# Optimization experiments

Measured on AMD Instinct MI355X. Metric: run time of the kernel, lower is better.

Reference implementation:

```python
import jax, jax.numpy as jnp
import numpy as np

B, D, C = 4096, 128, 256


def setup_inputs() -> dict:
    key = jax.random.key(0)
    kx, km, kc = jax.random.split(key, 3)
    X = jax.random.normal(kx, (B, D), dtype=jnp.float32)
    means = jax.random.normal(km, (D, C), dtype=jnp.float32)
    # Build an SPD covariance and invert it (as the torch module does in __init__)
    A = jax.random.normal(kc, (D, D), dtype=jnp.float32)
    covar = A @ A.T / D + jnp.eye(D, dtype=jnp.float32)
    alpha = jnp.linalg.inv(covar)  # [D, D]
    return {"X": X, "means": means, "alpha": alpha}


def reference(X, means, alpha):
    # X: [B, D], means: [D, C], alpha: [D, D]
    d2 = X[:, :, None] - means[None, :, :]          # [B, D, C]
    # Quadratic form diagonal only: q[b,c] = d2[b,:,c]^T alpha d2[b,:,c]
    ad2 = jnp.einsum('de,bec->bdc', alpha, d2)       # [B, D, C]
    q = jnp.einsum('bdc,bdc->bc', d2, ad2)           # [B, C]
    return jnp.min(q, axis=1)                        # [B]
```

## Files before the change

### kernel.cpp

```cpp
#include <hip/hip_runtime.h>
#include <hip/hip_bf16.h>

constexpr int Bn = 4096;
constexpr int Dn = 128;
constexpr int Cn = 256;

typedef __attribute__((ext_vector_type(8))) short bf16x8;
typedef __attribute__((ext_vector_type(4))) float f32x4;

static __device__ inline unsigned short f2bfu(float f) {
    __hip_bfloat16 h = __float2bfloat16(f);
    return *reinterpret_cast<unsigned short*>(&h);
}
static __device__ inline float bfu2f(unsigned short u) {
    __hip_bfloat16 h = *reinterpret_cast<__hip_bfloat16*>(&u);
    return __bfloat162float(h);
}
static __device__ inline unsigned pk2(float x, float y) {
    return (unsigned)f2bfu(x) | ((unsigned)f2bfu(y) << 16);
}

#define SWZ_OFF(row, e) ((row) * 256 + ((((e) * 2)) ^ (((row) & 7) << 4)))

__global__ __launch_bounds__(512) void fused_kernel(
    const float* __restrict__ X, const float* __restrict__ means,
    const float* __restrict__ alpha, float* __restrict__ out) {
    __shared__ __align__(16) unsigned char AL[Dn * 256];
    __shared__ __align__(16) unsigned char MT[Cn * 256];
    __shared__ __align__(16) unsigned char XL[16 * 256];
    __shared__ float SMIN[8][16];
    __shared__ float SXAX[8][16];

    const int tid = threadIdx.x;
    const int w = tid >> 6;
    const int lane = tid & 63;
    const int l15 = lane & 15;
    const int lh = lane >> 4;
    const int b0 = blockIdx.x * 16;

    {
        {
            float4 v = ((const float4*)(X + b0 * Dn))[tid];
            const int b = tid >> 5;
            const int e0 = (tid & 31) << 2;
            uint2 pk;
            pk.x = pk2(v.x, v.y); pk.y = pk2(v.z, v.w);
            *(uint2*)(XL + SWZ_OFF(b, e0)) = pk;
        }
        const float4* a4 = (const float4*)alpha;
        #pragma unroll
        for (int i = 0; i < 8; ++i) {
            int idx4 = tid + i * 512;
            int d = idx4 >> 5, e0 = (idx4 & 31) << 2;
            float4 v = a4[idx4];
            unsigned char* p = AL + SWZ_OFF(d, e0);
            *(unsigned*)p = pk2(v.x, v.y);
            *(unsigned*)(p + 4) = pk2(v.z, v.w);
        }
        const int cb = 8 * w + (lane & 7);
        const int db0 = lane >> 3;
        #pragma unroll
        for (int i = 0; i < 4; ++i) {
            const int db = db0 + 8 * i;
            float4 v0 = *(const float4*)&means[(4 * db + 0) * Cn + 4 * cb];
            float4 v1 = *(const float4*)&means[(4 * db + 1) * Cn + 4 * cb];
            float4 v2 = *(const float4*)&means[(4 * db + 2) * Cn + 4 * cb];
            float4 v3 = *(const float4*)&means[(4 * db + 3) * Cn + 4 * cb];
            uint2 pk;
            pk.x = pk2(v0.x, v1.x); pk.y = pk2(v2.x, v3.x);
            *(uint2*)(MT + SWZ_OFF(4 * cb + 0, 4 * db)) = pk;
            pk.x = pk2(v0.y, v1.y); pk.y = pk2(v2.y, v3.y);
            *(uint2*)(MT + SWZ_OFF(4 * cb + 1, 4 * db)) = pk;
            pk.x = pk2(v0.z, v1.z); pk.y = pk2(v2.z, v3.z);
            *(uint2*)(MT + SWZ_OFF(4 * cb + 2, 4 * db)) = pk;
            pk.x = pk2(v0.w, v1.w); pk.y = pk2(v2.w, v3.w);
            *(uint2*)(MT + SWZ_OFF(4 * cb + 3, 4 * db)) = pk;
        }
    }
    __syncthreads();

    f32x4 gacc[2][8];
    #pragma unroll
    for (int j = 0; j < 2; ++j)
        #pragma unroll
        for (int mt = 0; mt < 8; ++mt) gacc[j][mt] = (f32x4){0.f, 0.f, 0.f, 0.f};
    f32x4 xacc = (f32x4){0.f, 0.f, 0.f, 0.f};

    #pragma unroll
    for (int k0 = 0; k0 < 4; ++k0) {
        bf16x8 bj[2];
        #pragma unroll
        for (int j = 0; j < 2; ++j) {
            const int c = 32 * w + 16 * j + l15;
            bj[j] = *(const bf16x8*)(MT + SWZ_OFF(c, 32 * k0 + 8 * lh));
        }
        #pragma unroll
        for (int mt = 0; mt < 8; ++mt) {
            bf16x8 a = *(const bf16x8*)(AL + SWZ_OFF(16 * mt + l15, 32 * k0 + 8 * lh));
            #pragma unroll
            for (int j = 0; j < 2; ++j)
                gacc[j][mt] = __builtin_amdgcn_mfma_f32_16x16x32_bf16(a, bj[j], gacc[j][mt], 0, 0, 0);
        }
        {
            bf16x8 a = *(const bf16x8*)(AL + SWZ_OFF(16 * w + l15, 32 * k0 + 8 * lh));
            bf16x8 bx = *(const bf16x8*)(XL + SWZ_OFF(l15, 32 * k0 + 8 * lh));
            xacc = __builtin_amdgcn_mfma_f32_16x16x32_bf16(a, bx, xacc, 0, 0, 0);
        }
    }

    {
        uint2 pk = *(const uint2*)(XL + SWZ_OFF(l15, 16 * w + 4 * lh));
        float v = bfu2f((unsigned short)(pk.x & 0xffffu)) * xacc[0];
        v = fmaf(bfu2f((unsigned short)(pk.x >> 16)),     xacc[1], v);
        v = fmaf(bfu2f((unsigned short)(pk.y & 0xffffu)), xacc[2], v);
        v = fmaf(bfu2f((unsigned short)(pk.y >> 16)),     xacc[3], v);
        v += __shfl_xor(v, 16);
        v += __shfl_xor(v, 32);
        if (lane < 16) SXAX[w][lane] = v;
    }

    float tp[2];
    #pragma unroll
    for (int j = 0; j < 2; ++j) {
        const int c = 32 * w + 16 * j + l15;
        float v = 0.f;
        #pragma unroll
        for (int mt = 0; mt < 8; ++mt) {
            uint2 pk = *(const uint2*)(MT + SWZ_OFF(c, 16 * mt + 4 * lh));
            v = fmaf(bfu2f((unsigned short)(pk.x & 0xffffu)), gacc[j][mt][0], v);
            v = fmaf(bfu2f((unsigned short)(pk.x >> 16)),     gacc[j][mt][1], v);
            v = fmaf(bfu2f((unsigned short)(pk.y & 0xffffu)), gacc[j][mt][2], v);
            v = fmaf(bfu2f((unsigned short)(pk.y >> 16)),     gacc[j][mt][3], v);
        }
        v += __shfl_xor(v, 16);
        v += __shfl_xor(v, 32);
        tp[j] = v;
    }

    #pragma unroll
    for (int j = 0; j < 2; ++j) {
        const int c = 32 * w + 16 * j + l15;
        #pragma unroll
        for (int mt = 0; mt < 8; ++mt) {
            uint2 pk;
            pk.x = pk2(gacc[j][mt][0], gacc[j][mt][1]);
            pk.y = pk2(gacc[j][mt][2], gacc[j][mt][3]);
            *(uint2*)(MT + SWZ_OFF(c, 16 * mt + 4 * lh)) = pk;
        }
    }
    __syncthreads();

    bf16x8 af[4];
    #pragma unroll
    for (int k0 = 0; k0 < 4; ++k0)
        af[k0] = *(const bf16x8*)(XL + SWZ_OFF(l15, 32 * k0 + 8 * lh));
    bf16x8 bf2[2][4];
    #pragma unroll
    for (int j2 = 0; j2 < 2; ++j2) {
        const int rowc = 16 * (2 * w + j2) + l15;
        #pragma unroll
        for (int k0 = 0; k0 < 4; ++k0)
            bf2[j2][k0] = *(const bf16x8*)(MT + SWZ_OFF(rowc, 32 * k0 + 8 * lh));
    }
    f32x4 macc[2];
    #pragma unroll
    for (int j2 = 0; j2 < 2; ++j2) macc[j2] = (f32x4){0.f, 0.f, 0.f, 0.f};
    #pragma unroll
    for (int k0 = 0; k0 < 4; ++k0)
        #pragma unroll
        for (int j2 = 0; j2 < 2; ++j2)
            macc[j2] = __builtin_amdgcn_mfma_f32_16x16x32_bf16(af[k0], bf2[j2][k0], macc[j2], 0, 0, 0);

    {
        float mr[4];
        #pragma unroll
        for (int r = 0; r < 4; ++r) mr[r] = 1e30f;
        #pragma unroll
        for (int j2 = 0; j2 < 2; ++j2) {
            const float tc = tp[j2];
            #pragma unroll
            for (int r = 0; r < 4; ++r)
                mr[r] = fminf(mr[r], tc - 2.f * macc[j2][r]);
        }
        #pragma unroll
        for (int r = 0; r < 4; ++r) {
            #pragma unroll
            for (int m = 1; m < 16; m <<= 1)
                mr[r] = fminf(mr[r], __shfl_xor(mr[r], m));
        }
        if (l15 == 0)
            #pragma unroll
            for (int r = 0; r < 4; ++r) SMIN[w][4 * lh + r] = mr[r];
    }
    __syncthreads();

    if (tid < 16) {
        float mnv = 1e30f, xa = 0.f;
        #pragma unroll
        for (int w8 = 0; w8 < 8; ++w8) {
            mnv = fminf(mnv, SMIN[w8][tid]);
            xa += SXAX[w8][tid];
        }
        out[b0 + tid] = xa + mnv;
    }
}

extern "C" void kernel_launch(void* const* d_in, const int* in_sizes, int n_in,
                              void* d_out, int out_size, void* d_ws, size_t ws_size,
                              hipStream_t stream) {
    const float* X     = (const float*)d_in[0];
    const float* means = (const float*)d_in[1];
    const float* alpha = (const float*)d_in[2];
    float* out = (float*)d_out;
    fused_kernel<<<Bn / 16, 512, 0, stream>>>(X, means, alpha, out);
}
```

Baseline: 11.73 us.

## Retile alpha*means GEMM into 2x4 warp grid with partial-sum reduction via LDS

Splits the first GEMM's output tile across waves as 2 row groups by 4 column groups (64 columns x 64 rows per wave) instead of each wave owning 32 columns and all 128 rows. Each wave now issues fewer A-fragment LDS loads per MFMA because each A fragment is reused across four B fragments. The per-column quadratic term becomes a partial sum per row group, combined through a new shared TP buffer. This adds an extra __syncthreads. The X fragments are also loaded once and reused for both the xacc MFMA and the final GEMM.

```diff
diff --git a/kernel.cpp b/kernel.cpp
--- a/kernel.cpp
+++ b/kernel.cpp
@@ -28,6 +28,7 @@
     __shared__ __align__(16) unsigned char AL[Dn * 256];
     __shared__ __align__(16) unsigned char MT[Cn * 256];
     __shared__ __align__(16) unsigned char XL[16 * 256];
+    __shared__ float TP[2][Cn];
     __shared__ float SMIN[8][16];
     __shared__ float SXAX[8][16];
 
@@ -37,6 +38,8 @@
     const int l15 = lane & 15;
     const int lh = lane >> 4;
     const int b0 = blockIdx.x * 16;
+    const int cg = w & 3;
+    const int rg = w >> 2;
 
     {
         {
@@ -79,32 +82,34 @@
     }
     __syncthreads();
 
-    f32x4 gacc[2][8];
-    #pragma unroll
-    for (int j = 0; j < 2; ++j)
-        #pragma unroll
-        for (int mt = 0; mt < 8; ++mt) gacc[j][mt] = (f32x4){0.f, 0.f, 0.f, 0.f};
+    f32x4 gacc[4][4];
+    #pragma unroll
+    for (int j = 0; j < 4; ++j)
+        #pragma unroll
+        for (int s = 0; s < 4; ++s) gacc[j][s] = (f32x4){0.f, 0.f, 0.f, 0.f};
     f32x4 xacc = (f32x4){0.f, 0.f, 0.f, 0.f};
+    bf16x8 af[4];
 
     #pragma unroll
     for (int k0 = 0; k0 < 4; ++k0) {
-        bf16x8 bj[2];
-        #pragma unroll
-        for (int j = 0; j < 2; ++j) {
-            const int c = 32 * w + 16 * j + l15;
+        af[k0] = *(const bf16x8*)(XL + SWZ_OFF(l15, 32 * k0 + 8 * lh));
+        bf16x8 bj[4];
+        #pragma unroll
+        for (int j = 0; j < 4; ++j) {
+            const int c = 64 * cg + 16 * j + l15;
             bj[j] = *(const bf16x8*)(MT + SWZ_OFF(c, 32 * k0 + 8 * lh));
         }
         #pragma unroll
-        for (int mt = 0; mt < 8; ++mt) {
+        for (int s = 0; s < 4; ++s) {
+            const int mt = 4 * rg + s;
             bf16x8 a = *(const bf16x8*)(AL + SWZ_OFF(16 * mt + l15, 32 * k0 + 8 * lh));
             #pragma unroll
-            for (int j = 0; j < 2; ++j)
-                gacc[j][mt] = __builtin_amdgcn_mfma_f32_16x16x32_bf16(a, bj[j], gacc[j][mt], 0, 0, 0);
+            for (int j = 0; j < 4; ++j)
+                gacc[j][s] = __builtin_amdgcn_mfma_f32_16x16x32_bf16(a, bj[j], gacc[j][s], 0, 0, 0);
         }
         {
-            bf16x8 a = *(const bf16x8*)(AL + SWZ_OFF(16 * w + l15, 32 * k0 + 8 * lh));
-            bf16x8 bx = *(const bf16x8*)(XL + SWZ_OFF(l15, 32 * k0 + 8 * lh));
-            xacc = __builtin_amdgcn_mfma_f32_16x16x32_bf16(a, bx, xacc, 0, 0, 0);
+            bf16x8 aH = *(const bf16x8*)(AL + SWZ_OFF(16 * w + l15, 32 * k0 + 8 * lh));
+            xacc = __builtin_amdgcn_mfma_f32_16x16x32_bf16(aH, af[k0], xacc, 0, 0, 0);
         }
     }
 
@@ -119,41 +124,45 @@
         if (lane < 16) SXAX[w][lane] = v;
     }
 
-    float tp[2];
-    #pragma unroll
-    for (int j = 0; j < 2; ++j) {
-        const int c = 32 * w + 16 * j + l15;
-        float v = 0.f;
-        #pragma unroll
-        for (int mt = 0; mt < 8; ++mt) {
-            uint2 pk = *(const uint2*)(MT + SWZ_OFF(c, 16 * mt + 4 * lh));
-            v = fmaf(bfu2f((unsigned short)(pk.x & 0xffffu)), gacc[j][mt][0], v);
-            v = fmaf(bfu2f((unsigned short)(pk.x >> 16)),     gacc[j][mt][1], v);
-            v = fmaf(bfu2f((unsigned short)(pk.y & 0xffffu)), gacc[j][mt][2], v);
-            v = fmaf(bfu2f((unsigned short)(pk.y >> 16)),     gacc[j][mt][3], v);
-        }
-        v += __shfl_xor(v, 16);
-        v += __shfl_xor(v, 32);
-        tp[j] = v;
-    }
-
-    #pragma unroll
-    for (int j = 0; j < 2; ++j) {
-        const int c = 32 * w + 16 * j + l15;
-        #pragma unroll
-        for (int mt = 0; mt < 8; ++mt) {
+    {
+        float tpart[4];
+        #pragma unroll
+        for (int j = 0; j < 4; ++j) {
+            const int c = 64 * cg + 16 * j + l15;
+            float v = 0.f;
+            #pragma unroll
+            for (int s = 0; s < 4; ++s) {
+                const int mt = 4 * rg + s;
+                uint2 mm = *(const uint2*)(MT + SWZ_OFF(c, 16 * mt + 4 * lh));
+                v = fmaf(bfu2f((unsigned short)(mm.x & 0xffffu)), gacc[j][s][0], v);
+                v = fmaf(bfu2f((unsigned short)(mm.x >> 16)),     gacc[j][s][1], v);
+                v = fmaf(bfu2f((unsigned short)(mm.y & 0xffffu)), gacc[j][s][2], v);
+                v = fmaf(bfu2f((unsigned short)(mm.y >> 16)),     gacc[j][s][3], v);
+            }
+            v += __shfl_xor(v, 16);
+            v += __shfl_xor(v, 32);
+            tpart[j] = v;
+        }
+        if (lane < 16)
+            #pragma unroll
+            for (int j = 0; j < 4; ++j) TP[rg][64 * cg + 16 * j + lane] = tpart[j];
+    }
+    __syncthreads();
+
+    #pragma unroll
+    for (int j = 0; j < 4; ++j) {
+        const int c = 64 * cg + 16 * j + l15;
+        #pragma unroll
+        for (int s = 0; s < 4; ++s) {
+            const int mt = 4 * rg + s;
             uint2 pk;
-            pk.x = pk2(gacc[j][mt][0], gacc[j][mt][1]);
-            pk.y = pk2(gacc[j][mt][2], gacc[j][mt][3]);
+            pk.x = pk2(gacc[j][s][0], gacc[j][s][1]);
+            pk.y = pk2(gacc[j][s][2], gacc[j][s][3]);
             *(uint2*)(MT + SWZ_OFF(c, 16 * mt + 4 * lh)) = pk;
         }
     }
     __syncthreads();
 
-    bf16x8 af[4];
-    #pragma unroll
-    for (int k0 = 0; k0 < 4; ++k0)
-        af[k0] = *(const bf16x8*)(XL + SWZ_OFF(l15, 32 * k0 + 8 * lh));
     bf16x8 bf2[2][4];
     #pragma unroll
     for (int j2 = 0; j2 < 2; ++j2) {
@@ -177,7 +186,8 @@
         for (int r = 0; r < 4; ++r) mr[r] = 1e30f;
         #pragma unroll
         for (int j2 = 0; j2 < 2; ++j2) {
-            const float tc = tp[j2];
+            const int c = 16 * (2 * w + j2) + l15;
+            const float tc = TP[0][c] + TP[1][c];
             #pragma unroll
             for (int r = 0; r < 4; ++r)
                 mr[r] = fminf(mr[r], tc - 2.f * macc[j2][r]);
```

Result: no change. 11.51 us (-1.8%).
